# Kernel tuning notes

Measured on AMD Instinct MI355X. Metric: run time of the kernel, lower is better.

## Reference

```python
import jax, jax.numpy as jnp
import numpy as np

N_NODES = 100000
N_EDGES = 1600000
IN_CH = 128
HID = 128
OUT_CH = 40


def setup_inputs() -> dict:
    key = jax.random.key(0)
    ks = jax.random.split(key, 8)
    x = jax.random.normal(ks[0], (N_NODES, IN_CH), dtype=jnp.float32)
    edge_index = jax.random.randint(ks[1], (2, N_EDGES), 0, N_NODES, dtype=jnp.int64)
    s1 = 1.0 / np.sqrt(IN_CH)
    s2 = 1.0 / np.sqrt(HID)
    # SAGEConv layer 1: lin_l (applied to aggregated neighbors, has bias), lin_r (applied to root, no bias)
    Wl1 = jax.random.uniform(ks[2], (IN_CH, HID), jnp.float32, -s1, s1)
    b1 = jnp.zeros((HID,), jnp.float32)
    Wr1 = jax.random.uniform(ks[3], (IN_CH, HID), jnp.float32, -s1, s1)
    # SAGEConv layer 2
    Wl2 = jax.random.uniform(ks[4], (HID, OUT_CH), jnp.float32, -s2, s2)
    b2 = jnp.zeros((OUT_CH,), jnp.float32)
    Wr2 = jax.random.uniform(ks[5], (HID, OUT_CH), jnp.float32, -s2, s2)
    return {"x": x, "edge_index": edge_index, "Wl1": Wl1, "b1": b1, "Wr1": Wr1,
            "Wl2": Wl2, "b2": b2, "Wr2": Wr2}


def _sage_conv(x, src, dst, Wl, b, Wr):
    # mean-aggregate source-node features onto target nodes (PyG SAGEConv, aggr='mean')
    msg_sum = jax.ops.segment_sum(x[src], dst, num_segments=N_NODES)  # [N, F]
    deg = jax.ops.segment_sum(jnp.ones((src.shape[0],), x.dtype), dst, num_segments=N_NODES)
    aggr = msg_sum / jnp.maximum(deg, 1.0)[:, None]
    return aggr @ Wl + b + x @ Wr


def reference(x, edge_index, Wl1, b1, Wr1, Wl2, b2, Wr2):
    src, dst = edge_index[0], edge_index[1]
    h = _sage_conv(x, src, dst, Wl1, b1, Wr1)
    h = jax.nn.relu(h)  # dropout is identity in eval mode
    h = _sage_conv(h, src, dst, Wl2, b2, Wr2)
    return jax.nn.log_softmax(h, axis=-1)
```

## Files before the change

### kernel.cpp

```cpp
#include <hip/hip_runtime.h>
#include <math.h>

#define NN 100000
#define NE 1600000
#define NBUK ((NN + 255) / 256)
#define CAP 5120
#define NBLK_A 500
#define EPB (NE / NBLK_A)
#define GPB (EPB / 4)
#define MT ((NN + 127) / 128)
#define MPAD ((size_t)MT * 128)
#define NT2 (NN / 16)
#define PACK_B 192
#define CVT_B0 (NBLK_A + PACK_B)
#define FRONT_GRID 2048

typedef __attribute__((ext_vector_type(8))) short short8;
typedef __attribute__((ext_vector_type(4))) float f32x4;
typedef __attribute__((ext_vector_type(4))) int i32x4;
typedef unsigned short ushort_t;
typedef unsigned int uint_t;

__device__ inline ushort_t f2bf(float f) {
    uint_t u = __builtin_bit_cast(uint_t, f);
    u += 0x7FFFu + ((u >> 16) & 1u);
    return (ushort_t)(u >> 16);
}
__device__ inline float bits2f(uint_t u) { return __builtin_bit_cast(float, u); }
__device__ inline float lo16(uint_t u) { return bits2f(u << 16); }
__device__ inline float hi16(uint_t u) { return bits2f(u & 0xFFFF0000u); }

__device__ inline void gload_lds16(const void* g, void* l) {
    __builtin_amdgcn_global_load_lds(
        (const __attribute__((address_space(1))) unsigned int*)g,
        (__attribute__((address_space(3))) unsigned int*)l, 16, 0, 0);
}

__global__ __launch_bounds__(256) void front(const float* __restrict__ x,
                                             ushort_t* __restrict__ xb,
                                             const float* __restrict__ Wl1,
                                             const float* __restrict__ Wr1,
                                             const float* __restrict__ Wl2,
                                             const float* __restrict__ Wr2,
                                             ushort_t* __restrict__ W1T,
                                             ushort_t* __restrict__ W2T,
                                             const int* __restrict__ ei,
                                             int* __restrict__ bhist,
                                             int* __restrict__ bhp) {
    __shared__ int h[NBUK];
    int bid = blockIdx.x, tid = threadIdx.x;
    if (bid < NBLK_A) {
        for (int i = tid; i < NBUK; i += 256) h[i] = 0;
        __syncthreads();
        const i32x4* dsts = (const i32x4*)(ei + NE + bid * EPB);
        for (int g = tid; g < GPB; g += 256) {
            i32x4 d = __builtin_nontemporal_load(dsts + g);
#pragma unroll
            for (int j = 0; j < 4; ++j) atomicAdd(&h[d[j] >> 8], 1);
        }
        __syncthreads();
        for (int i = tid; i < NBUK; i += 256) {
            int c = h[i];
            bhp[bid * NBUK + i] = c;
            if (c) atomicAdd(&bhist[i], c);
        }
    } else if (bid < CVT_B0) {
        int gid = (bid - NBLK_A) * 256 + tid;
        if (gid < 256 * 128) {
            int n = gid >> 7, k = gid & 127;
            float v = (n < 128) ? Wl1[k * 128 + n] : Wr1[k * 128 + (n - 128)];
            W1T[gid] = f2bf(v);
        } else {
            int g = gid - 256 * 128;
            if (g < 128 * 128) {
                int n = g >> 7, k = g & 127;
                float v = 0.0f;
                if (n < 40)      v = Wl2[k * 40 + n];
                else if (n < 80) v = Wr2[k * 40 + (n - 40)];
                W2T[g] = f2bf(v);
            }
        }
    } else {
        const int total = NN * 128 / 8;
        const int nb = FRONT_GRID - CVT_B0;
        const f32x4* src = (const f32x4*)x;
        for (int g = (bid - CVT_B0) * 256 + tid; g < total; g += nb * 256) {
            f32x4 v0 = __builtin_nontemporal_load(src + (size_t)g * 2);
            f32x4 v1 = __builtin_nontemporal_load(src + (size_t)g * 2 + 1);
            i32x4 o;
            o[0] = ((uint_t)f2bf(v0[1]) << 16) | (uint_t)f2bf(v0[0]);
            o[1] = ((uint_t)f2bf(v0[3]) << 16) | (uint_t)f2bf(v0[2]);
            o[2] = ((uint_t)f2bf(v1[1]) << 16) | (uint_t)f2bf(v1[0]);
            o[3] = ((uint_t)f2bf(v1[3]) << 16) | (uint_t)f2bf(v1[2]);
            *(i32x4*)(xb + (size_t)g * 8) = o;
        }
    }
}

__global__ __launch_bounds__(512) void scan_buckets(const int* __restrict__ bhist,
                                                    int* __restrict__ boff,
                                                    int* __restrict__ gcur,
                                                    int* __restrict__ offsets) {
    __shared__ int part[512];
    int t = threadIdx.x;
    int v = (t < NBUK) ? bhist[t] : 0;
    part[t] = v;
    __syncthreads();
    for (int d = 1; d < 512; d <<= 1) {
        int tmp = (t >= d) ? part[t - d] : 0;
        __syncthreads();
        part[t] += tmp;
        __syncthreads();
    }
    if (t <= NBUK) {
        int excl = (t == 0) ? 0 : part[t - 1];
        boff[t] = excl;
        if (t < NBUK) gcur[t] = excl;
    }
    if (t == 0) offsets[NN] = NE;
}

__global__ __launch_bounds__(256) void bin_pass(const int* __restrict__ ei,
                                                const int* __restrict__ bhp,
                                                int* __restrict__ gcur,
                                                int* __restrict__ pairs) {
    __shared__ int h[NBUK];
    __shared__ int base[NBUK];
    int bid = blockIdx.x, tid = threadIdx.x;
    const int* myh = bhp + bid * NBUK;
    for (int i = tid; i < NBUK; i += 256) {
        int c = myh[i];
        base[i] = c ? atomicAdd(&gcur[i], c) : 0;
        h[i] = 0;
    }
    __syncthreads();
    int e0 = bid * EPB;
    const i32x4* dsts = (const i32x4*)(ei + NE + e0);
    const i32x4* srcs = (const i32x4*)(ei + e0);
    for (int g = tid; g < GPB; g += 256) {
        i32x4 d = __builtin_nontemporal_load(dsts + g);
        i32x4 s = __builtin_nontemporal_load(srcs + g);
#pragma unroll
        for (int j = 0; j < 4; ++j) {
            int buk = d[j] >> 8;
            int pos = base[buk] + atomicAdd(&h[buk], 1);
            pairs[pos] = (s[j] << 8) | (d[j] & 255);
        }
    }
}

__global__ __launch_bounds__(256) void sort_buckets(const int* __restrict__ boff,
                                                    const int* __restrict__ pairs,
                                                    int* __restrict__ offsets,
                                                    int* __restrict__ ssrc) {
    __shared__ int plds[CAP];
    __shared__ int slds[CAP];
    __shared__ int cnt[256];
    __shared__ int excl[256];
    int buk = blockIdx.x, tid = threadIdx.x;
    int bstart = boff[buk], bend = boff[buk + 1];
    int count = min(bend - bstart, CAP);
    int lo = buk << 8;
    cnt[tid] = 0;
    __syncthreads();
    for (int j = tid; j < count; j += 256) {
        int p = pairs[bstart + j];
        plds[j] = p;
        atomicAdd(&cnt[p & 255], 1);
    }
    __syncthreads();
    int c = cnt[tid];
    excl[tid] = c;
    __syncthreads();
    for (int d = 1; d < 256; d <<= 1) {
        int tmp = (tid >= d) ? excl[tid - d] : 0;
        __syncthreads();
        excl[tid] += tmp;
        __syncthreads();
    }
    int myExcl = excl[tid] - c;
    __syncthreads();
    excl[tid] = myExcl;
    cnt[tid] = 0;
    __syncthreads();
    for (int j = tid; j < count; j += 256) {
        int p = plds[j];
        int loc = p & 255;
        int pos = excl[loc] + atomicAdd(&cnt[loc], 1);
        slds[pos] = p >> 8;
    }
    __syncthreads();
    for (int j = tid; j < count; j += 256) ssrc[bstart + j] = slds[j];
    if (lo + tid < NN) offsets[lo + tid] = bstart + myExcl;
}

__global__ __launch_bounds__(256, 2) void gemm_mfma(const ushort_t* __restrict__ A,
                                                    const ushort_t* __restrict__ Bt,
                                                    ushort_t* __restrict__ G,
                                                    ushort_t* __restrict__ Croot,
                                                    int M, int split, int rootEnd, int gstride) {
    __shared__ __align__(16) char As[128 * 256];
    __shared__ __align__(16) char Bs[128 * 256];
    int tid = threadIdx.x;
    int lane = tid & 63, wid = tid >> 6;
    int quad = lane >> 4, l15 = lane & 15;
    int wm = (wid & 1) * 64, wn = (wid >> 1) * 64;
    int mBase = blockIdx.x * 128, nBase = blockIdx.y * 128;
    int rootW = rootEnd - split;

    const char* aT = (const char*)(A + (size_t)mBase * 128);
    const char* bT = (const char*)(Bt + (size_t)nBase * 128);
#pragma unroll
    for (int ii = 0; ii < 8; ++ii) {
        int rr = (wid * 8 + ii) * 4 + quad;
        int src = rr * 256 + ((l15 * 16) ^ ((rr & 7) << 4));
        int ldsb = (wid * 8 + ii) * 1024;
        gload_lds16(aT + src, As + ldsb);
        gload_lds16(bT + src, Bs + ldsb);
    }
    asm volatile("s_waitcnt vmcnt(0)" ::: "memory");
    __syncthreads();

    f32x4 acc[4][4];
#pragma unroll
    for (int i = 0; i < 4; ++i)
#pragma unroll
        for (int j = 0; j < 4; ++j) acc[i][j] = (f32x4){0.f, 0.f, 0.f, 0.f};

#pragma unroll
    for (int kk = 0; kk < 4; ++kk) {
        int kByte = kk * 64 + quad * 16;
        short8 af[4], bfr[4];
#pragma unroll
        for (int i = 0; i < 4; ++i) {
            int row = wm + i * 16 + l15;
            af[i] = *(const short8*)(As + row * 256 + (kByte ^ ((row & 7) << 4)));
        }
#pragma unroll
        for (int j = 0; j < 4; ++j) {
            int row = wn + j * 16 + l15;
            bfr[j] = *(const short8*)(Bs + row * 256 + (kByte ^ ((row & 7) << 4)));
        }
#pragma unroll
        for (int i = 0; i < 4; ++i)
#pragma unroll
            for (int j = 0; j < 4; ++j)
                acc[i][j] = __builtin_amdgcn_mfma_f32_16x16x32_bf16(af[i], bfr[j],
                                                                    acc[i][j], 0, 0, 0);
    }

#pragma unroll
    for (int i = 0; i < 4; ++i) {
#pragma unroll
        for (int r = 0; r < 4; ++r) {
            int m = mBase + wm + i * 16 + quad * 4 + r;
            if (m >= M) continue;
#pragma unroll
            for (int j = 0; j < 4; ++j) {
                int n = nBase + wn + j * 16 + l15;
                float v = acc[i][j][r];
                if (n < split) G[(size_t)m * gstride + n] = f2bf(v);
                else if (n < rootEnd) Croot[(size_t)m * rootW + (n - split)] = f2bf(v);
            }
        }
    }
}

__global__ __launch_bounds__(256) void agg1_gemm2(const int* __restrict__ offsets,
                                                  const int* __restrict__ ssrc,
                                                  const ushort_t* __restrict__ G1,
                                                  const ushort_t* __restrict__ C1root,
                                                  const float* __restrict__ b1,
                                                  const ushort_t* __restrict__ W2T,
                                                  ushort_t* __restrict__ G2,
                                                  ushort_t* __restrict__ C2root) {
    __shared__ __align__(16) char stage[4][16 * 256];
    int tid = threadIdx.x, lane = tid & 63, wid = tid >> 6;
    int g = lane >> 4, q = lane & 15;
    int qb = q << 4;
    int t = blockIdx.x * 4 + wid;
    int m0 = t * 16;
    char* sw = stage[wid];
    const char* Gb = (const char*)G1;

    for (int pass = 0; pass < 16; ++pass) {
        int w = m0 + pass;
        if (w < NN) {
            int start = offsets[w], end = offsets[w + 1];
            float a0 = 0.f, a1 = 0.f, a2 = 0.f, a3 = 0.f,
                  a4 = 0.f, a5 = 0.f, a6 = 0.f, a7 = 0.f;
            for (int base = start; base < end; base += 64) {
                int cnt = min(64, end - base);
                int idx = (base + lane < end) ? ssrc[base + lane] : 0;
                int j = 0;
                for (; j + 16 <= cnt; j += 16) {
                    int s0 = __shfl(idx, j + g, 64);
                    int s1 = __shfl(idx, j + 4 + g, 64);
                    int s2 = __shfl(idx, j + 8 + g, 64);
                    int s3 = __shfl(idx, j + 12 + g, 64);
                    uint4 u0 = *(const uint4*)(Gb + (s0 << 8) + qb);
                    uint4 u1 = *(const uint4*)(Gb + (s1 << 8) + qb);
                    uint4 u2 = *(const uint4*)(Gb + (s2 << 8) + qb);
                    uint4 u3 = *(const uint4*)(Gb + (s3 << 8) + qb);
                    a0 += (lo16(u0.x) + lo16(u1.x)) + (lo16(u2.x) + lo16(u3.x));
                    a1 += (hi16(u0.x) + hi16(u1.x)) + (hi16(u2.x) + hi16(u3.x));
                    a2 += (lo16(u0.y) + lo16(u1.y)) + (lo16(u2.y) + lo16(u3.y));
                    a3 += (hi16(u0.y) + hi16(u1.y)) + (hi16(u2.y) + hi16(u3.y));
                    a4 += (lo16(u0.z) + lo16(u1.z)) + (lo16(u2.z) + lo16(u3.z));
                    a5 += (hi16(u0.z) + hi16(u1.z)) + (hi16(u2.z) + hi16(u3.z));
                    a6 += (lo16(u0.w) + lo16(u1.w)) + (lo16(u2.w) + lo16(u3.w));
                    a7 += (hi16(u0.w) + hi16(u1.w)) + (hi16(u2.w) + hi16(u3.w));
                }
                for (; j + 8 <= cnt; j += 8) {
                    int s0 = __shfl(idx, j + g, 64);
                    int s1 = __shfl(idx, j + 4 + g, 64);
                    uint4 u0 = *(const uint4*)(Gb + (s0 << 8) + qb);
                    uint4 u1 = *(const uint4*)(Gb + (s1 << 8) + qb);
                    a0 += lo16(u0.x) + lo16(u1.x);
                    a1 += hi16(u0.x) + hi16(u1.x);
                    a2 += lo16(u0.y) + lo16(u1.y);
                    a3 += hi16(u0.y) + hi16(u1.y);
                    a4 += lo16(u0.z) + lo16(u1.z);
                    a5 += hi16(u0.z) + hi16(u1.z);
                    a6 += lo16(u0.w) + lo16(u1.w);
                    a7 += hi16(u0.w) + hi16(u1.w);
                }
                for (; j < cnt; j += 4) {
                    int e = j + g;
                    int s0 = __shfl(idx, (e < cnt) ? e : 0, 64);
                    if (e < cnt) {
                        uint4 u0 = *(const uint4*)(Gb + (s0 << 8) + qb);
                        a0 += lo16(u0.x); a1 += hi16(u0.x);
                        a2 += lo16(u0.y); a3 += hi16(u0.y);
                        a4 += lo16(u0.z); a5 += hi16(u0.z);
                        a6 += lo16(u0.w); a7 += hi16(u0.w);
                    }
                }
            }
            a0 += __shfl_xor(a0, 16, 64); a0 += __shfl_xor(a0, 32, 64);
            a1 += __shfl_xor(a1, 16, 64); a1 += __shfl_xor(a1, 32, 64);
            a2 += __shfl_xor(a2, 16, 64); a2 += __shfl_xor(a2, 32, 64);
            a3 += __shfl_xor(a3, 16, 64); a3 += __shfl_xor(a3, 32, 64);
            a4 += __shfl_xor(a4, 16, 64); a4 += __shfl_xor(a4, 32, 64);
            a5 += __shfl_xor(a5, 16, 64); a5 += __shfl_xor(a5, 32, 64);
            a6 += __shfl_xor(a6, 16, 64); a6 += __shfl_xor(a6, 32, 64);
            a7 += __shfl_xor(a7, 16, 64); a7 += __shfl_xor(a7, 32, 64);
            if (g == 0) {
                float inv = 1.0f / fmaxf((float)(end - start), 1.0f);
                uint4 rv = *(const uint4*)((const char*)C1root + (size_t)w * 256 + qb);
                float4 c0 = *(const float4*)(b1 + q * 8);
                float4 c1 = *(const float4*)(b1 + q * 8 + 4);
                float h0 = fmaxf(a0 * inv + c0.x + lo16(rv.x), 0.f);
                float h1 = fmaxf(a1 * inv + c0.y + hi16(rv.x), 0.f);
                float h2 = fmaxf(a2 * inv + c0.z + lo16(rv.y), 0.f);
                float h3 = fmaxf(a3 * inv + c0.w + hi16(rv.y), 0.f);
                float h4 = fmaxf(a4 * inv + c1.x + lo16(rv.z), 0.f);
                float h5 = fmaxf(a5 * inv + c1.y + hi16(rv.z), 0.f);
                float h6 = fmaxf(a6 * inv + c1.z + lo16(rv.w), 0.f);
                float h7 = fmaxf(a7 * inv + c1.w + hi16(rv.w), 0.f);
                uint4 o;
                o.x = ((uint_t)f2bf(h1) << 16) | (uint_t)f2bf(h0);
                o.y = ((uint_t)f2bf(h3) << 16) | (uint_t)f2bf(h2);
                o.z = ((uint_t)f2bf(h5) << 16) | (uint_t)f2bf(h4);
                o.w = ((uint_t)f2bf(h7) << 16) | (uint_t)f2bf(h6);
                *(uint4*)(sw + pass * 256 + ((q ^ (pass & 7)) << 4)) = o;
            }
        }
    }
    __syncthreads();
    if (m0 >= NN) return;

    int quad = g, l15 = q;
    f32x4 acc[5];
#pragma unroll
    for (int j = 0; j < 5; ++j) acc[j] = (f32x4){0.f, 0.f, 0.f, 0.f};
#pragma unroll
    for (int kk = 0; kk < 4; ++kk) {
        int cu = kk * 4 + quad;
        short8 af = *(const short8*)(sw + l15 * 256 + ((cu ^ (l15 & 7)) << 4));
#pragma unroll
        for (int j = 0; j < 5; ++j) {
            short8 bfr = *(const short8*)(W2T + (size_t)(j * 16 + l15) * 128 + kk * 32 + quad * 8);
            acc[j] = __builtin_amdgcn_mfma_f32_16x16x32_bf16(af, bfr, acc[j], 0, 0, 0);
        }
    }
#pragma unroll
    for (int j = 0; j < 5; ++j) {
#pragma unroll
        for (int r = 0; r < 4; ++r) {
            int m = m0 + quad * 4 + r;
            int n = j * 16 + l15;
            float v = acc[j][r];
            if (n < 40) G2[(size_t)m * 64 + n] = f2bf(v);
            else if (n < 80) C2root[(size_t)m * 40 + (n - 40)] = f2bf(v);
        }
    }
}

__global__ __launch_bounds__(256) void aggregate2(const int* __restrict__ offsets,
                                                  const int* __restrict__ ssrc,
                                                  const ushort_t* __restrict__ G2,
                                                  const ushort_t* __restrict__ C2root,
                                                  const float* __restrict__ b2,
                                                  float* __restrict__ out) {
    int w = (blockIdx.x * blockDim.x + threadIdx.x) >> 6;
    int lane = threadIdx.x & 63;
    if (w >= NN) return;
    int start = offsets[w], end = offsets[w + 1];
    int g = lane >> 4, q = lane & 15;
    bool act = q < 10;
    int qb = q << 3;
    const char* Gb = (const char*)G2;
    float a0 = 0.f, a1 = 0.f, a2 = 0.f, a3 = 0.f;
    for (int base = start; base < end; base += 64) {
        int cnt = min(64, end - base);
        int idx = (base + lane < end) ? ssrc[base + lane] : 0;
        int j = 0;
        for (; j + 16 <= cnt; j += 16) {
            int s0 = __shfl(idx, j + g, 64);
            int s1 = __shfl(idx, j + 4 + g, 64);
            int s2 = __shfl(idx, j + 8 + g, 64);
            int s3 = __shfl(idx, j + 12 + g, 64);
            if (act) {
                uint2 u0 = *(const uint2*)(Gb + (s0 << 7) + qb);
                uint2 u1 = *(const uint2*)(Gb + (s1 << 7) + qb);
                uint2 u2 = *(const uint2*)(Gb + (s2 << 7) + qb);
                uint2 u3 = *(const uint2*)(Gb + (s3 << 7) + qb);
                a0 += (lo16(u0.x) + lo16(u1.x)) + (lo16(u2.x) + lo16(u3.x));
                a1 += (hi16(u0.x) + hi16(u1.x)) + (hi16(u2.x) + hi16(u3.x));
                a2 += (lo16(u0.y) + lo16(u1.y)) + (lo16(u2.y) + lo16(u3.y));
                a3 += (hi16(u0.y) + hi16(u1.y)) + (hi16(u2.y) + hi16(u3.y));
            }
        }
        for (; j + 8 <= cnt; j += 8) {
            int s0 = __shfl(idx, j + g, 64);
            int s1 = __shfl(idx, j + 4 + g, 64);
            if (act) {
                uint2 u0 = *(const uint2*)(Gb + (s0 << 7) + qb);
                uint2 u1 = *(const uint2*)(Gb + (s1 << 7) + qb);
                a0 += lo16(u0.x) + lo16(u1.x);
                a1 += hi16(u0.x) + hi16(u1.x);
                a2 += lo16(u0.y) + lo16(u1.y);
                a3 += hi16(u0.y) + hi16(u1.y);
            }
        }
        for (; j < cnt; j += 4) {
            int e = j + g;
            int s0 = __shfl(idx, (e < cnt) ? e : 0, 64);
            if (act && e < cnt) {
                uint2 u0 = *(const uint2*)(Gb + (s0 << 7) + qb);
                a0 += lo16(u0.x); a1 += hi16(u0.x);
                a2 += lo16(u0.y); a3 += hi16(u0.y);
            }
        }
    }
    a0 += __shfl_xor(a0, 16, 64); a0 += __shfl_xor(a0, 32, 64);
    a1 += __shfl_xor(a1, 16, 64); a1 += __shfl_xor(a1, 32, 64);
    a2 += __shfl_xor(a2, 16, 64); a2 += __shfl_xor(a2, 32, 64);
    a3 += __shfl_xor(a3, 16, 64); a3 += __shfl_xor(a3, 32, 64);
    if (g == 0) {
        float inv = 1.0f / fmaxf((float)(end - start), 1.0f);
        float v0 = -INFINITY, v1 = -INFINITY, v2 = -INFINITY, v3 = -INFINITY;
        if (act) {
            uint2 rv = *(const uint2*)((const char*)C2root + (size_t)w * 80 + qb);
            float4 bb = *(const float4*)(b2 + q * 4);
            v0 = a0 * inv + bb.x + lo16(rv.x);
            v1 = a1 * inv + bb.y + hi16(rv.x);
            v2 = a2 * inv + bb.z + lo16(rv.y);
            v3 = a3 * inv + bb.w + hi16(rv.y);
        }
        float m = fmaxf(fmaxf(v0, v1), fmaxf(v2, v3));
#pragma unroll
        for (int d = 8; d >= 1; d >>= 1) m = fmaxf(m, __shfl_xor(m, d, 64));
        float e = act ? (expf(v0 - m) + expf(v1 - m)) + (expf(v2 - m) + expf(v3 - m)) : 0.f;
#pragma unroll
        for (int d = 8; d >= 1; d >>= 1) e += __shfl_xor(e, d, 64);
        float lse = m + logf(e);
        if (act) {
            float4 o = make_float4(v0 - lse, v1 - lse, v2 - lse, v3 - lse);
            *(float4*)(out + (size_t)w * 40 + q * 4) = o;
        }
    }
}

extern "C" void kernel_launch(void* const* d_in, const int* in_sizes, int n_in,
                              void* d_out, int out_size, void* d_ws, size_t ws_size,
                              hipStream_t stream) {
    const float* x   = (const float*)d_in[0];
    const int*   ei  = (const int*)d_in[1];
    const float* Wl1 = (const float*)d_in[2];
    const float* b1  = (const float*)d_in[3];
    const float* Wr1 = (const float*)d_in[4];
    const float* Wl2 = (const float*)d_in[5];
    const float* b2  = (const float*)d_in[6];
    const float* Wr2 = (const float*)d_in[7];
    float* out = (float*)d_out;

    char* ws = (char*)d_ws;
    size_t off = 0;
    auto alloc = [&](size_t bytes) -> void* {
        void* p = ws + off;
        off = (off + bytes + 255) & ~(size_t)255;
        return p;
    };
    int*      bhist   = (int*)alloc((size_t)NBUK * 4);
    int*      boff    = (int*)alloc((size_t)(NBUK + 1) * 4);
    int*      gcur    = (int*)alloc((size_t)NBUK * 4);
    int*      bhp     = (int*)alloc((size_t)NBLK_A * NBUK * 4);
    int*      pairs   = (int*)alloc((size_t)NE * 4);
    int*      offsets = (int*)alloc((size_t)(NN + 1) * 4);
    int*      ssrc    = (int*)alloc((size_t)NE * 4);
    ushort_t* W1T     = (ushort_t*)alloc((size_t)256 * 128 * 2);
    ushort_t* W2T     = (ushort_t*)alloc((size_t)128 * 128 * 2);
    ushort_t* xb      = (ushort_t*)alloc(MPAD * 128 * 2);
    ushort_t* G1      = (ushort_t*)alloc((size_t)NN * 128 * 2);
    ushort_t* C1root  = (ushort_t*)alloc((size_t)NN * 128 * 2);
    ushort_t* G2      = (ushort_t*)alloc((size_t)NN * 64 * 2);
    ushort_t* C2root  = (ushort_t*)alloc((size_t)NN * 40 * 2);

    hipMemsetAsync(bhist, 0, (size_t)NBUK * 4, stream);

    front<<<FRONT_GRID, 256, 0, stream>>>(x, xb, Wl1, Wr1, Wl2, Wr2, W1T, W2T, ei, bhist, bhp);
    scan_buckets<<<1, 512, 0, stream>>>(bhist, boff, gcur, offsets);
    bin_pass<<<NBLK_A, 256, 0, stream>>>(ei, bhp, gcur, pairs);
    sort_buckets<<<NBUK, 256, 0, stream>>>(boff, pairs, offsets, ssrc);

    dim3 g1(MT, 2);
    gemm_mfma<<<g1, 256, 0, stream>>>(xb, W1T, G1, C1root, NN, 128, 256, 128);

    agg1_gemm2<<<(NT2 + 3) / 4, 256, 0, stream>>>(offsets, ssrc, G1, C1root, b1, W2T, G2, C2root);

    aggregate2<<<(NN * 64 + 255) / 256, 256, 0, stream>>>(offsets, ssrc, G2, C2root, b2, out);
}
```

Baseline: 352.7 us.

## Chunk layer-1 features by column for cache-local gathers and split agg1/gemm2

The layer-1 GEMM now writes its neighbour-transformed output in a column-chunked layout (8 chunks of 16 features per node). A new aggregate kernel processes one chunk per block, so each gather touches a 3.2MB slice that can stay in cache rather than the full feature table. The fused aggregate+GEMM2 kernel is replaced by a separate chunked aggregation that writes a chunked hidden tensor, followed by a reuse of the MFMA GEMM kernel with chunked A input. This costs an extra launch and a round trip of the hidden activations through memory. Each node's edge indices are also re-read once per chunk.

Result: slower. 367.6 us (+4.2%).

```diff
diff --git a/kernel.cpp b/kernel.cpp
--- a/kernel.cpp
+++ b/kernel.cpp
@@ -10,10 +10,11 @@
 #define GPB (EPB / 4)
 #define MT ((NN + 127) / 128)
 #define MPAD ((size_t)MT * 128)
-#define NT2 (NN / 16)
 #define PACK_B 192
 #define CVT_B0 (NBLK_A + PACK_B)
 #define FRONT_GRID 2048
+#define AGG1_BG 1563
+#define AGG1_GRID (AGG1_BG * 8)
 
 typedef __attribute__((ext_vector_type(8))) short short8;
 typedef __attribute__((ext_vector_type(4))) float f32x4;
@@ -194,9 +195,9 @@
     if (lo + tid < NN) offsets[lo + tid] = bstart + myExcl;
 }
 
-__global__ __launch_bounds__(256, 2) void gemm_mfma(const ushort_t* __restrict__ A,
+__global__ __launch_bounds__(256, 2) void gemm_mfma(const ushort_t* __restrict__ A, int aChunked,
                                                     const ushort_t* __restrict__ Bt,
-                                                    ushort_t* __restrict__ G,
+                                                    ushort_t* __restrict__ G, int gChunked,
                                                     ushort_t* __restrict__ Croot,
                                                     int M, int split, int rootEnd, int gstride) {
     __shared__ __align__(16) char As[128 * 256];
@@ -208,15 +209,18 @@
     int mBase = blockIdx.x * 128, nBase = blockIdx.y * 128;
     int rootW = rootEnd - split;
 
-    const char* aT = (const char*)(A + (size_t)mBase * 128);
+    const char* aBase = (const char*)A;
     const char* bT = (const char*)(Bt + (size_t)nBase * 128);
 #pragma unroll
     for (int ii = 0; ii < 8; ++ii) {
         int rr = (wid * 8 + ii) * 4 + quad;
-        int src = rr * 256 + ((l15 * 16) ^ ((rr & 7) << 4));
+        int cb = (l15 * 16) ^ ((rr & 7) << 4);
+        const char* srcA = aChunked
+            ? aBase + (((size_t)(cb >> 5) * MPAD + (mBase + rr)) << 5) + (cb & 31)
+            : aBase + (size_t)(mBase + rr) * 256 + cb;
         int ldsb = (wid * 8 + ii) * 1024;
-        gload_lds16(aT + src, As + ldsb);
-        gload_lds16(bT + src, Bs + ldsb);
+        gload_lds16(srcA, As + ldsb);
+        gload_lds16(bT + rr * 256 + cb, Bs + ldsb);
     }
     asm volatile("s_waitcnt vmcnt(0)" ::: "memory");
     __syncthreads();
@@ -259,141 +263,65 @@
             for (int j = 0; j < 4; ++j) {
                 int n = nBase + wn + j * 16 + l15;
                 float v = acc[i][j][r];
-                if (n < split) G[(size_t)m * gstride + n] = f2bf(v);
-                else if (n < rootEnd) Croot[(size_t)m * rootW + (n - split)] = f2bf(v);
-            }
-        }
-    }
-}
-
-__global__ __launch_bounds__(256) void agg1_gemm2(const int* __restrict__ offsets,
-                                                  const int* __restrict__ ssrc,
-                                                  const ushort_t* __restrict__ G1,
-                                                  const ushort_t* __restrict__ C1root,
-                                                  const float* __restrict__ b1,
-                                                  const ushort_t* __restrict__ W2T,
-                                                  ushort_t* __restrict__ G2,
-                                                  ushort_t* __restrict__ C2root) {
-    __shared__ __align__(16) char stage[4][16 * 256];
-    int tid = threadIdx.x, lane = tid & 63, wid = tid >> 6;
-    int g = lane >> 4, q = lane & 15;
-    int qb = q << 4;
-    int t = blockIdx.x * 4 + wid;
-    int m0 = t * 16;
-    char* sw = stage[wid];
-    const char* Gb = (const char*)G1;
-
-    for (int pass = 0; pass < 16; ++pass) {
-        int w = m0 + pass;
-        if (w < NN) {
-            int start = offsets[w], end = offsets[w + 1];
-            float a0 = 0.f, a1 = 0.f, a2 = 0.f, a3 = 0.f,
-                  a4 = 0.f, a5 = 0.f, a6 = 0.f, a7 = 0.f;
-            for (int base = start; base < end; base += 64) {
-                int cnt = min(64, end - base);
-                int idx = (base + lane < end) ? ssrc[base + lane] : 0;
-                int j = 0;
-                for (; j + 16 <= cnt; j += 16) {
-                    int s0 = __shfl(idx, j + g, 64);
-                    int s1 = __shfl(idx, j + 4 + g, 64);
-                    int s2 = __shfl(idx, j + 8 + g, 64);
-                    int s3 = __shfl(idx, j + 12 + g, 64);
-                    uint4 u0 = *(const uint4*)(Gb + (s0 << 8) + qb);
-                    uint4 u1 = *(const uint4*)(Gb + (s1 << 8) + qb);
-                    uint4 u2 = *(const uint4*)(Gb + (s2 << 8) + qb);
-                    uint4 u3 = *(const uint4*)(Gb + (s3 << 8) + qb);
-                    a0 += (lo16(u0.x) + lo16(u1.x)) + (lo16(u2.x) + lo16(u3.x));
-                    a1 += (hi16(u0.x) + hi16(u1.x)) + (hi16(u2.x) + hi16(u3.x));
-                    a2 += (lo16(u0.y) + lo16(u1.y)) + (lo16(u2.y) + lo16(u3.y));
-                    a3 += (hi16(u0.y) + hi16(u1.y)) + (hi16(u2.y) + hi16(u3.y));
-                    a4 += (lo16(u0.z) + lo16(u1.z)) + (lo16(u2.z) + lo16(u3.z));
-                    a5 += (hi16(u0.z) + hi16(u1.z)) + (hi16(u2.z) + hi16(u3.z));
-                    a6 += (lo16(u0.w) + lo16(u1.w)) + (lo16(u2.w) + lo16(u3.w));
-                    a7 += (hi16(u0.w) + hi16(u1.w)) + (hi16(u2.w) + hi16(u3.w));
-                }
-                for (; j + 8 <= cnt; j += 8) {
-                    int s0 = __shfl(idx, j + g, 64);
-                    int s1 = __shfl(idx, j + 4 + g, 64);
-                    uint4 u0 = *(const uint4*)(Gb + (s0 << 8) + qb);
-                    uint4 u1 = *(const uint4*)(Gb + (s1 << 8) + qb);
-                    a0 += lo16(u0.x) + lo16(u1.x);
-                    a1 += hi16(u0.x) + hi16(u1.x);
-                    a2 += lo16(u0.y) + lo16(u1.y);
-                    a3 += hi16(u0.y) + hi16(u1.y);
-                    a4 += lo16(u0.z) + lo16(u1.z);
-                    a5 += hi16(u0.z) + hi16(u1.z);
-                    a6 += lo16(u0.w) + lo16(u1.w);
-                    a7 += hi16(u0.w) + hi16(u1.w);
-                }
-                for (; j < cnt; j += 4) {
-                    int e = j + g;
-                    int s0 = __shfl(idx, (e < cnt) ? e : 0, 64);
-                    if (e < cnt) {
-                        uint4 u0 = *(const uint4*)(Gb + (s0 << 8) + qb);
-                        a0 += lo16(u0.x); a1 += hi16(u0.x);
-                        a2 += lo16(u0.y); a3 += hi16(u0.y);
-                        a4 += lo16(u0.z); a5 += hi16(u0.z);
-                        a6 += lo16(u0.w); a7 += hi16(u0.w);
-                    }
+                if (n < split) {
+                    size_t go = gChunked ? (((size_t)(n >> 4) * NN + m) * 16 + (n & 15))
+                                         : ((size_t)m * gstride + n);
+                    G[go] = f2bf(v);
+                } else if (n < rootEnd) {
+                    Croot[(size_t)m * rootW + (n - split)] = f2bf(v);
                 }
             }
-            a0 += __shfl_xor(a0, 16, 64); a0 += __shfl_xor(a0, 32, 64);
-            a1 += __shfl_xor(a1, 16, 64); a1 += __shfl_xor(a1, 32, 64);
-            a2 += __shfl_xor(a2, 16, 64); a2 += __shfl_xor(a2, 32, 64);
-            a3 += __shfl_xor(a3, 16, 64); a3 += __shfl_xor(a3, 32, 64);
-            a4 += __shfl_xor(a4, 16, 64); a4 += __shfl_xor(a4, 32, 64);
-            a5 += __shfl_xor(a5, 16, 64); a5 += __shfl_xor(a5, 32, 64);
-            a6 += __shfl_xor(a6, 16, 64); a6 += __shfl_xor(a6, 32, 64);
-            a7 += __shfl_xor(a7, 16, 64); a7 += __shfl_xor(a7, 32, 64);
-            if (g == 0) {
-                float inv = 1.0f / fmaxf((float)(end - start), 1.0f);
-                uint4 rv = *(const uint4*)((const char*)C1root + (size_t)w * 256 + qb);
-                float4 c0 = *(const float4*)(b1 + q * 8);
-                float4 c1 = *(const float4*)(b1 + q * 8 + 4);
-                float h0 = fmaxf(a0 * inv + c0.x + lo16(rv.x), 0.f);
-                float h1 = fmaxf(a1 * inv + c0.y + hi16(rv.x), 0.f);
-                float h2 = fmaxf(a2 * inv + c0.z + lo16(rv.y), 0.f);
-                float h3 = fmaxf(a3 * inv + c0.w + hi16(rv.y), 0.f);
-                float h4 = fmaxf(a4 * inv + c1.x + lo16(rv.z), 0.f);
-                float h5 = fmaxf(a5 * inv + c1.y + hi16(rv.z), 0.f);
-                float h6 = fmaxf(a6 * inv + c1.z + lo16(rv.w), 0.f);
-                float h7 = fmaxf(a7 * inv + c1.w + hi16(rv.w), 0.f);
-                uint4 o;
-                o.x = ((uint_t)f2bf(h1) << 16) | (uint_t)f2bf(h0);
-                o.y = ((uint_t)f2bf(h3) << 16) | (uint_t)f2bf(h2);
-                o.z = ((uint_t)f2bf(h5) << 16) | (uint_t)f2bf(h4);
-                o.w = ((uint_t)f2bf(h7) << 16) | (uint_t)f2bf(h6);
-                *(uint4*)(sw + pass * 256 + ((q ^ (pass & 7)) << 4)) = o;
-            }
-        }
-    }
-    __syncthreads();
-    if (m0 >= NN) return;
-
-    int quad = g, l15 = q;
-    f32x4 acc[5];
-#pragma unroll
-    for (int j = 0; j < 5; ++j) acc[j] = (f32x4){0.f, 0.f, 0.f, 0.f};
-#pragma unroll
-    for (int kk = 0; kk < 4; ++kk) {
-        int cu = kk * 4 + quad;
-        short8 af = *(const short8*)(sw + l15 * 256 + ((cu ^ (l15 & 7)) << 4));
-#pragma unroll
-        for (int j = 0; j < 5; ++j) {
-            short8 bfr = *(const short8*)(W2T + (size_t)(j * 16 + l15) * 128 + kk * 32 + quad * 8);
-            acc[j] = __builtin_amdgcn_mfma_f32_16x16x32_bf16(af, bfr, acc[j], 0, 0, 0);
-        }
-    }
-#pragma unroll
-    for (int j = 0; j < 5; ++j) {
-#pragma unroll
-        for (int r = 0; r < 4; ++r) {
-            int m = m0 + quad * 4 + r;
-            int n = j * 16 + l15;
-            float v = acc[j][r];
-            if (n < 40) G2[(size_t)m * 64 + n] = f2bf(v);
-            else if (n < 80) C2root[(size_t)m * 40 + (n - 40)] = f2bf(v);
-        }
+        }
+    }
+}
+
+__global__ __launch_bounds__(256) void aggregate1c(const int* __restrict__ offsets,
+                                                   const int* __restrict__ ssrc,
+                                                   const ushort_t* __restrict__ G1c,
+                                                   const ushort_t* __restrict__ C1root,
+                                                   const float* __restrict__ b1,
+                                                   ushort_t* __restrict__ s1bc) {
+    int tid = threadIdx.x, lane = tid & 63, wid = tid >> 6;
+    int bid = blockIdx.x;
+    int chunk = bid & 7;
+    int bg = bid >> 3;
+    int ns = lane >> 2, cpart = lane & 3;
+    int w = (bg * 4 + wid) * 16 + ns;
+    bool alive = w < NN;
+    int start = 0, end = 0;
+    if (alive) { start = offsets[w]; end = offsets[w + 1]; }
+    const char* Gb = (const char*)G1c + (size_t)chunk * NN * 32 + cpart * 8;
+    float a0 = 0.f, a1 = 0.f, a2 = 0.f, a3 = 0.f;
+    int e = start;
+    for (; e + 4 <= end; e += 4) {
+        int i0 = ssrc[e], i1 = ssrc[e + 1], i2 = ssrc[e + 2], i3 = ssrc[e + 3];
+        uint2 u0 = *(const uint2*)(Gb + (size_t)i0 * 32);
+        uint2 u1 = *(const uint2*)(Gb + (size_t)i1 * 32);
+        uint2 u2 = *(const uint2*)(Gb + (size_t)i2 * 32);
+        uint2 u3 = *(const uint2*)(Gb + (size_t)i3 * 32);
+        a0 += (lo16(u0.x) + lo16(u1.x)) + (lo16(u2.x) + lo16(u3.x));
+        a1 += (hi16(u0.x) + hi16(u1.x)) + (hi16(u2.x) + hi16(u3.x));
+        a2 += (lo16(u0.y) + lo16(u1.y)) + (lo16(u2.y) + lo16(u3.y));
+        a3 += (hi16(u0.y) + hi16(u1.y)) + (hi16(u2.y) + hi16(u3.y));
+    }
+    for (; e < end; ++e) {
+        int i0 = ssrc[e];
+        uint2 u0 = *(const uint2*)(Gb + (size_t)i0 * 32);
+        a0 += lo16(u0.x); a1 += hi16(u0.x);
+        a2 += lo16(u0.y); a3 += hi16(u0.y);
+    }
+    if (alive) {
+        float inv = 1.0f / fmaxf((float)(end - start), 1.0f);
+        uint2 rv = *(const uint2*)((const char*)C1root + (size_t)w * 256 + chunk * 32 + cpart * 8);
+        float4 bb = *(const float4*)(b1 + chunk * 16 + cpart * 4);
+        float h0 = fmaxf(a0 * inv + bb.x + lo16(rv.x), 0.f);
+        float h1 = fmaxf(a1 * inv + bb.y + hi16(rv.x), 0.f);
+        float h2 = fmaxf(a2 * inv + bb.z + lo16(rv.y), 0.f);
+        float h3 = fmaxf(a3 * inv + bb.w + hi16(rv.y), 0.f);
+        uint2 o;
+        o.x = ((uint_t)f2bf(h1) << 16) | (uint_t)f2bf(h0);
+        o.y = ((uint_t)f2bf(h3) << 16) | (uint_t)f2bf(h2);
+        *(uint2*)((char*)s1bc + ((size_t)chunk * MPAD + w) * 32 + cpart * 8) = o;
     }
 }
 
@@ -513,8 +441,9 @@
     ushort_t* W1T     = (ushort_t*)alloc((size_t)256 * 128 * 2);
     ushort_t* W2T     = (ushort_t*)alloc((size_t)128 * 128 * 2);
     ushort_t* xb      = (ushort_t*)alloc(MPAD * 128 * 2);
-    ushort_t* G1      = (ushort_t*)alloc((size_t)NN * 128 * 2);
+    ushort_t* G1c     = (ushort_t*)alloc((size_t)8 * NN * 16 * 2);
     ushort_t* C1root  = (ushort_t*)alloc((size_t)NN * 128 * 2);
+    ushort_t* s1bc    = (ushort_t*)alloc((size_t)8 * MPAD * 16 * 2);
     ushort_t* G2      = (ushort_t*)alloc((size_t)NN * 64 * 2);
     ushort_t* C2root  = (ushort_t*)alloc((size_t)NN * 40 * 2);
 
@@ -526,9 +455,12 @@
     sort_buckets<<<NBUK, 256, 0, stream>>>(boff, pairs, offsets, ssrc);
 
     dim3 g1(MT, 2);
-    gemm_mfma<<<g1, 256, 0, stream>>>(xb, W1T, G1, C1root, NN, 128, 256, 128);
-
-    agg1_gemm2<<<(NT2 + 3) / 4, 256, 0, stream>>>(offsets, ssrc, G1, C1root, b1, W2T, G2, C2root);
+    gemm_mfma<<<g1, 256, 0, stream>>>(xb, 0, W1T, G1c, 1, C1root, NN, 128, 256, 0);
+
+    aggregate1c<<<AGG1_GRID, 256, 0, stream>>>(offsets, ssrc, G1c, C1root, b1, s1bc);
+
+    dim3 g2(MT, 1);
+    gemm_mfma<<<g2, 256, 0, stream>>>(s1bc, 1, W2T, G2, 0, C2root, NN, 40, 80, 64);
 
     aggregate2<<<(NN * 64 + 255) / 256, 256, 0, stream>>>(offsets, ssrc, G2, C2root, b2, out);
 }
```
